# Performance work log

Measured on AMD Instinct MI355X. Metric: run time of the kernel, lower is better.

Reference implementation:

```python
import jax, jax.numpy as jnp
import numpy as np


def _extract_patches(x, k):
    # tf.image.extract_patches(sizes=[1,k,k,1], strides=1, rates=1, padding='SAME')
    # reshaped to [B,H,W,k*k,C]; window ordered row-major (di, dj), zero padded.
    B, H, W, C = x.shape
    p = k // 2
    xp = jnp.pad(x, ((0, 0), (p, p), (p, p), (0, 0)))
    # fixed k*k=25 shifted views; stacking along new patch axis
    views = [xp[:, i:i + H, j:j + W, :] for i in range(k) for j in range(k)]
    return jnp.stack(views, axis=3)  # [B,H,W,k*k,C]


def reference(main, main_value, ref, ref_value, k_size=5):
    # main/ref: [B,H,W,C]; main_value/ref_value: [B,H,W,V]
    ref_p = _extract_patches(ref, k_size)            # [B,H,W,K,C], K=k*k
    refv_p = _extract_patches(ref_value, k_size)     # [B,H,W,K,V]

    # scores for the K neighbor slots plus one self slot (main concat at end)
    scores_nbr = jnp.einsum('bhwkc,bhwc->bhwk', ref_p, main)   # [B,H,W,K]
    score_self = jnp.einsum('bhwc,bhwc->bhw', main, main)      # [B,H,W]
    scores = jnp.concatenate([scores_nbr, score_self[..., None]], axis=-1)  # [B,H,W,K+1]

    attn = jax.nn.softmax(scores, axis=-1)                     # [B,H,W,K+1]

    values = jnp.concatenate([refv_p, main_value[:, :, :, None, :]], axis=3)  # [B,H,W,K+1,V]
    out = jnp.einsum('bhwk,bhwkv->bhwv', attn, values)         # [B,H,W,V]
    return out


def setup_inputs() -> dict:
    key = jax.random.key(0)
    k1, k2, k3, k4 = jax.random.split(key, 4)
    B, H, W, C, V = 2, 128, 128, 256, 64
    return {
        'main': jax.random.normal(k1, (B, H, W, C), dtype=jnp.float32),
        'main_value': jax.random.normal(k2, (B, H, W, V), dtype=jnp.float32),
        'ref': jax.random.normal(k3, (B, H, W, C), dtype=jnp.float32),
        'ref_value': jax.random.normal(k4, (B, H, W, V), dtype=jnp.float32),
    }
```

## Files before the change

### kernel.cpp

```cpp
#include <hip/hip_runtime.h>
#include <math.h>

namespace {

constexpr int Bn = 2, Hn = 128, Wn = 128, Cn = 256, Vn = 64;

__device__ __forceinline__ void load8(float* r, const float* p) {
    float4 a = *(const float4*)(p);
    float4 b = *(const float4*)(p + 4);
    r[0]=a.x; r[1]=a.y; r[2]=a.z; r[3]=a.w;
    r[4]=b.x; r[5]=b.y; r[6]=b.z; r[7]=b.w;
}

template <int CTRL>
__device__ __forceinline__ float row_add(float v) {
    int sh = __builtin_amdgcn_update_dpp(0, __float_as_int(v), CTRL, 0xF, 0xF, true);
    return v + __int_as_float(sh);
}

__device__ __forceinline__ float split_reduce(float v) {
    v = row_add<0xB1>(v);
    v = row_add<0x4E>(v);
    v = row_add<0x124>(v);
    v = row_add<0x128>(v);
    v += __int_as_float(__builtin_amdgcn_ds_swizzle(__float_as_int(v), 0x401F));
    return v;
}

__global__ __launch_bounds__(256)
void local_attn_kernel(const float* __restrict__ mainp,
                       const float* __restrict__ mainv,
                       const float* __restrict__ refp,
                       const float* __restrict__ refv,
                       float* __restrict__ outp)
{
    const int t = threadIdx.x;
    const int s = t & 31;
    const int g = t >> 5;
    const int blk = blockIdx.x;
    const int seg = blk & 7;
    const int h   = (blk >> 3) & (Hn - 1);
    const int b   = blk >> 10;
    const int w0  = seg * 16 + g * 2;
    const int rowbase = b * Hn + h;

    float m0[8], m1[8];
    const float* mp = mainp + ((size_t)rowbase * Wn + w0) * Cn + s * 8;
    load8(m0, mp);
    load8(m1, mp + Cn);

    float self0 = 0.f, self1 = 0.f;
    #pragma unroll
    for (int c = 0; c < 8; ++c) {
        self0 = fmaf(m0[c], m0[c], self0);
        self1 = fmaf(m1[c], m1[c], self1);
    }
    self0 = split_reduce(self0);
    self1 = split_reduce(self1);

    float mx0 = self0, mx1 = self1, den0 = 1.f, den1 = 1.f;
    float acc0[2], acc1[2];
    {
        const float* mvp = mainv + ((size_t)rowbase * Wn + w0) * Vn + s * 2;
        float2 a = *(const float2*)(mvp);
        float2 c = *(const float2*)(mvp + Vn);
        acc0[0] = a.x; acc0[1] = a.y;
        acc1[0] = c.x; acc1[1] = c.y;
    }

    #pragma unroll 1
    for (int di = 0; di < 5; ++di) {
        const int hh = h + di - 2;
        const bool rowok = (unsigned)hh < (unsigned)Hn;
        const size_t rbase = (size_t)(b * Hn + (rowok ? hh : 0)) * Wn;
        const float* rp = refp + rbase * Cn + s * 8;

        float sc0[5], sc1[5];
        #pragma unroll
        for (int o = 0; o < 6; ++o) {
            const int col = w0 - 2 + o;
            const bool ok = rowok && (unsigned)col < (unsigned)Wn;
            float r[8];
            #pragma unroll
            for (int c = 0; c < 8; ++c) r[c] = 0.f;
            if (ok) load8(r, rp + (size_t)col * Cn);
            if (o < 5) {
                float a = 0.f;
                #pragma unroll
                for (int c = 0; c < 8; ++c) a = fmaf(m0[c], r[c], a);
                sc0[o] = a;
            }
            if (o >= 1) {
                float a = 0.f;
                #pragma unroll
                for (int c = 0; c < 8; ++c) a = fmaf(m1[c], r[c], a);
                sc1[o - 1] = a;
            }
        }

        #pragma unroll
        for (int k = 0; k < 5; ++k) {
            sc0[k] = split_reduce(sc0[k]);
            sc1[k] = split_reduce(sc1[k]);
        }

        const float rm0 = fmaxf(fmaxf(fmaxf(sc0[0], sc0[1]), fmaxf(sc0[2], sc0[3])), sc0[4]);
        const float rm1 = fmaxf(fmaxf(fmaxf(sc1[0], sc1[1]), fmaxf(sc1[2], sc1[3])), sc1[4]);
        const float nm0 = fmaxf(mx0, rm0), nm1 = fmaxf(mx1, rm1);
        const float e0 = __expf(mx0 - nm0), e1 = __expf(mx1 - nm1);
        float sum0 = 0.f, sum1 = 0.f;
        #pragma unroll
        for (int k = 0; k < 5; ++k) {
            sc0[k] = __expf(sc0[k] - nm0); sum0 += sc0[k];
            sc1[k] = __expf(sc1[k] - nm1); sum1 += sc1[k];
        }
        den0 = den0 * e0 + sum0;
        den1 = den1 * e1 + sum1;
        acc0[0] *= e0; acc0[1] *= e0;
        acc1[0] *= e1; acc1[1] *= e1;
        mx0 = nm0; mx1 = nm1;

        const float* rvp = refv + rbase * Vn + s * 2;
        #pragma unroll
        for (int o = 0; o < 6; ++o) {
            const int col = w0 - 2 + o;
            float2 rv = make_float2(0.f, 0.f);
            if (rowok && (unsigned)col < (unsigned)Wn)
                rv = *(const float2*)(rvp + (size_t)col * Vn);
            if (o < 5) {
                const float wkj = sc0[o];
                acc0[0] = fmaf(wkj, rv.x, acc0[0]);
                acc0[1] = fmaf(wkj, rv.y, acc0[1]);
            }
            if (o >= 1) {
                const float wkj = sc1[o - 1];
                acc1[0] = fmaf(wkj, rv.x, acc1[0]);
                acc1[1] = fmaf(wkj, rv.y, acc1[1]);
            }
        }
    }

    const float inv0 = 1.f / den0, inv1 = 1.f / den1;
    float* op = outp + ((size_t)rowbase * Wn + w0) * Vn + s * 2;
    float2 o0, o1;
    o0.x = acc0[0] * inv0; o0.y = acc0[1] * inv0;
    o1.x = acc1[0] * inv1; o1.y = acc1[1] * inv1;
    *(float2*)(op)      = o0;
    *(float2*)(op + Vn) = o1;
}

}

extern "C" void kernel_launch(void* const* d_in, const int* in_sizes, int n_in,
                              void* d_out, int out_size, void* d_ws, size_t ws_size,
                              hipStream_t stream)
{
    const float* mainp = (const float*)d_in[0];
    const float* mainv = (const float*)d_in[1];
    const float* refp  = (const float*)d_in[2];
    const float* refv  = (const float*)d_in[3];
    float* outp = (float*)d_out;

    dim3 grid(Bn * Hn * 8);
    dim3 block(256);
    hipLaunchKernelGGL(local_attn_kernel, grid, block, 0, stream,
                       mainp, mainv, refp, refv, outp);
}
```

Baseline: 35.52 us.

## Stage per-row ref and ref_value tiles in shared memory for block reuse

Each block now loads the 20 ref columns (16 outputs plus halo) for the current window row into LDS cooperatively, with padded strides. Warps then read their 6 overlapping columns from LDS instead of issuing redundant global loads, which cuts global and L2 traffic from neighbouring warps re-reading the same columns. In exchange it adds two barriers per window row, an LDS round trip, and about 26KB of shared memory that can limit occupancy.

```diff
diff --git a/kernel.cpp b/kernel.cpp
--- a/kernel.cpp
+++ b/kernel.cpp
@@ -4,6 +4,8 @@
 namespace {
 
 constexpr int Bn = 2, Hn = 128, Wn = 128, Cn = 256, Vn = 64;
+constexpr int RS = 264;
+constexpr int VS = 66;
 
 __device__ __forceinline__ void load8(float* r, const float* p) {
     float4 a = *(const float4*)(p);
@@ -41,8 +43,12 @@
     const int seg = blk & 7;
     const int h   = (blk >> 3) & (Hn - 1);
     const int b   = blk >> 10;
-    const int w0  = seg * 16 + g * 2;
+    const int w0blk = seg * 16;
+    const int w0  = w0blk + g * 2;
     const int rowbase = b * Hn + h;
+
+    __shared__ float refS[20 * RS];
+    __shared__ float refVS[20 * VS];
 
     float m0[8], m1[8];
     const float* mp = mainp + ((size_t)rowbase * Wn + w0) * Cn + s * 8;
@@ -73,17 +79,43 @@
         const int hh = h + di - 2;
         const bool rowok = (unsigned)hh < (unsigned)Hn;
         const size_t rbase = (size_t)(b * Hn + (rowok ? hh : 0)) * Wn;
-        const float* rp = refp + rbase * Cn + s * 8;
+
+        if (di > 0) __syncthreads();
+
+        const float* rsrc = refp + rbase * Cn;
+        #pragma unroll
+        for (int i = 0; i < 5; ++i) {
+            const int idx = t + i * 256;
+            const int col = idx >> 6;
+            const int c4  = (idx & 63) << 2;
+            const int wcol = w0blk - 2 + col;
+            float4 v = make_float4(0.f, 0.f, 0.f, 0.f);
+            if (rowok && (unsigned)wcol < (unsigned)Wn)
+                v = *(const float4*)(rsrc + (size_t)wcol * Cn + c4);
+            *(float4*)(refS + col * RS + c4) = v;
+        }
+        const float* vsrc = refv + rbase * Vn;
+        #pragma unroll
+        for (int i = 0; i < 2; ++i) {
+            const int idx = t + i * 256;
+            if (idx < 320) {
+                const int col = idx >> 4;
+                const int c4  = (idx & 15) << 2;
+                const int wcol = w0blk - 2 + col;
+                float4 v = make_float4(0.f, 0.f, 0.f, 0.f);
+                if (rowok && (unsigned)wcol < (unsigned)Wn)
+                    v = *(const float4*)(vsrc + (size_t)wcol * Vn + c4);
+                *(float4*)(refVS + col * VS + c4) = v;
+            }
+        }
+        __syncthreads();
 
         float sc0[5], sc1[5];
         #pragma unroll
         for (int o = 0; o < 6; ++o) {
-            const int col = w0 - 2 + o;
-            const bool ok = rowok && (unsigned)col < (unsigned)Wn;
+            const float* cp = refS + (2 * g + o) * RS + s * 8;
             float r[8];
-            #pragma unroll
-            for (int c = 0; c < 8; ++c) r[c] = 0.f;
-            if (ok) load8(r, rp + (size_t)col * Cn);
+            load8(r, cp);
             if (o < 5) {
                 float a = 0.f;
                 #pragma unroll
@@ -120,13 +152,9 @@
         acc1[0] *= e1; acc1[1] *= e1;
         mx0 = nm0; mx1 = nm1;
 
-        const float* rvp = refv + rbase * Vn + s * 2;
         #pragma unroll
         for (int o = 0; o < 6; ++o) {
-            const int col = w0 - 2 + o;
-            float2 rv = make_float2(0.f, 0.f);
-            if (rowok && (unsigned)col < (unsigned)Wn)
-                rv = *(const float2*)(rvp + (size_t)col * Vn);
+            const float2 rv = *(const float2*)(refVS + (2 * g + o) * VS + s * 2);
             if (o < 5) {
                 const float wkj = sc0[o];
                 acc0[0] = fmaf(wkj, rv.x, acc0[0]);
```

Result: slower. 40.61 us (+14.3%).
